# Optimization experiments

Measured on AMD Instinct MI355X. Metric: run time of the kernel, lower is better.

## Reference

```python
import jax, jax.numpy as jnp
import numpy as np

MASK_NEG = 1e30


def setup_inputs() -> dict:
    key = jax.random.key(0)
    k_q, k_k, k_m, k_w1, k_w2, k_v = jax.random.split(key, 6)
    B, S, D, A = 32, 2048, 1024, 1024  # batch, seq, feature dim, attn dim
    # Xavier-uniform-like scale for weights
    lim = float(np.sqrt(6.0 / (D + A)))
    query = jax.random.normal(k_q, (B, D), dtype=jnp.float32)
    keys = jax.random.normal(k_k, (B, S, D), dtype=jnp.float32)
    mask = jax.random.randint(k_m, (B, S), 0, 2) > 0  # True = keep
    W1 = jax.random.uniform(k_w1, (A, D), jnp.float32, -lim, lim)
    W2 = jax.random.uniform(k_w2, (A, D), jnp.float32, -lim, lim)
    v = jax.random.uniform(k_v, (A,), jnp.float32, -lim, lim)
    return {"query": query, "keys": keys, "mask": mask, "W1": W1, "W2": W2, "v": v}


def reference(query, keys, mask, W1, W2, v):
    w1_query = jnp.einsum('bd,ad->ba', query, W1)          # (B, A)
    w2_keys = jnp.einsum('bsd,ad->bsa', keys, W2)          # (B, S, A)
    combined = jnp.tanh(w1_query[:, None, :] + w2_keys)    # (B, S, A)
    scores = jnp.einsum('bsa,a->bs', combined, v)          # (B, S)
    # masked softmax: subtract huge constant at masked-out positions
    scores = scores - (~mask).astype(scores.dtype) * MASK_NEG
    return jax.nn.softmax(scores, axis=-1)
```

## Files before the change

kernel.cpp:

```cpp
#include <hip/hip_runtime.h>
#include <hip/hip_bf16.h>
#include <stdint.h>

#define NB 32
#define NS 2048
#define ND 1024
#define NA 1024
#define MASK_NEG 1e30f

#define BM 256
#define BN 256
#define BK 64
#define NTILES 64

typedef __attribute__((ext_vector_type(4))) float f32x4;
typedef __attribute__((ext_vector_type(8))) __bf16 bf16x8;

__device__ __forceinline__ void glds16(const void* g, void* l) {
  __builtin_amdgcn_global_load_lds(
      (const __attribute__((address_space(1))) uint32_t*)g,
      (__attribute__((address_space(3))) uint32_t*)(uintptr_t)l, 16, 0, 0);
}

__global__ void zero_f32(float* __restrict__ p, int n) {
  int i = blockIdx.x * 256 + threadIdx.x;
  if (i < n) p[i] = 0.f;
}

__global__ __launch_bounds__(256) void cvt_bf16(const float* __restrict__ in,
                                                __bf16* __restrict__ out, int n8) {
  long i = blockIdx.x * 256 + threadIdx.x;
  const long stride = (long)gridDim.x * 256;
  for (; i < n8; i += stride) {
    f32x4 a = ((const f32x4*)in)[2 * i];
    f32x4 b = ((const f32x4*)in)[2 * i + 1];
    bf16x8 o;
#pragma unroll
    for (int j = 0; j < 4; ++j) { o[j] = (__bf16)a[j]; o[4 + j] = (__bf16)b[j]; }
    ((bf16x8*)out)[i] = o;
  }
}

__global__ __launch_bounds__(256) void w1q_kernel(const float* __restrict__ q,
                                                  const float* __restrict__ W1,
                                                  float* __restrict__ w1q) {
  const int b = blockIdx.x;
  const int a0 = blockIdx.y * 64;
  const int t = threadIdx.x;
  const int al = t >> 2;
  const int part = t & 3;
  const float* wrow = W1 + (size_t)(a0 + al) * ND + part * 256;
  const float* qrow = q + (size_t)b * ND + part * 256;
  float sum = 0.f;
#pragma unroll 8
  for (int i = 0; i < 256; i += 4) {
    float4 w = *reinterpret_cast<const float4*>(wrow + i);
    float4 x = *reinterpret_cast<const float4*>(qrow + i);
    sum += w.x * x.x + w.y * x.y + w.z * x.z + w.w * x.w;
  }
  __shared__ float red[256];
  red[t] = sum;
  __syncthreads();
  if (t < 64) {
    w1q[(size_t)b * NA + a0 + t] = red[t * 4] + red[t * 4 + 1] + red[t * 4 + 2] + red[t * 4 + 3];
  }
}

__global__ __launch_bounds__(512, 1) void score_gemm(
    const float* __restrict__ keysf, const __bf16* __restrict__ W2b,
    const float* __restrict__ w1q, const float* __restrict__ vvec,
    float* __restrict__ scores) {
  __shared__ __attribute__((aligned(1024))) char ldsA[6 * 16384];
  __shared__ __attribute__((aligned(1024))) char ldsB[4 * 16384];

  const int t = threadIdx.x;
  const int bs0 = blockIdx.x * BM;
  const int b = bs0 >> 11;
  const int lane = t & 63;
  const int wid = t >> 6;
  const int wr = wid >> 2;
  const int wc = wid & 3;
  const int lrow = lane & 15;
  const int ko = lane >> 4;

  const int rowA = t >> 4;
  const int scolA = (t & 15) ^ (rowA & 15);
  const int rowB = t >> 3;
  const int scolB = (t & 7) ^ (rowB & 7);

  const int uA0 = ko * 2, uA1 = 8 + ko * 2;
  const int sA00 = uA0 ^ lrow, sA01 = (uA0 + 1) ^ lrow;
  const int sA10 = uA1 ^ lrow, sA11 = (uA1 + 1) ^ lrow;
  const int sB0 = ko ^ (lrow & 7), sB1 = (4 + ko) ^ (lrow & 7);

  f32x4 acc[8][4];
#pragma unroll
  for (int mi = 0; mi < 8; ++mi)
#pragma unroll
    for (int ni = 0; ni < 4; ++ni) acc[mi][ni] = f32x4{0.f, 0.f, 0.f, 0.f};

  bf16x8 af[4][2], bfr[2][2];

#define STAGE_A(T, Q)                                                           \
  do {                                                                          \
    if ((T) < NTILES) {                                                         \
      const unsigned slot_ = (4u * (unsigned)(T) + (unsigned)(Q)) % 6u;         \
      char* d_ = ldsA + slot_ * 16384 + t * 16;                                 \
      const size_t r0_ = (size_t)(bs0 + (Q)*64 + rowA);                         \
      const int kf_ = ((T)&15) * 64 + scolA * 4;                                \
      glds16(keysf + r0_ * ND + kf_, d_);                                       \
      glds16(keysf + (r0_ + 32) * ND + kf_, d_ + 8192);                         \
    }                                                                           \
  } while (0)

#define STAGE_B(T, H)                                                           \
  do {                                                                          \
    if ((T) < NTILES) {                                                         \
      const unsigned slot_ = (2u * (unsigned)(T) + (unsigned)(H)) % 4u;         \
      char* d_ = ldsB + slot_ * 16384 + t * 16;                                 \
      const size_t r0_ = (size_t)(((T) >> 4) * 256 + (H)*128 + rowB);           \
      const int ke_ = (((T)&15) * 64) + scolB * 8;                              \
      glds16(W2b + r0_ * ND + ke_, d_);                                         \
      glds16(W2b + (r0_ + 64) * ND + ke_, d_ + 8192);                           \
    }                                                                           \
  } while (0)

#define SB_ __builtin_amdgcn_sched_barrier(0)
#define P1 __builtin_amdgcn_s_setprio(1)
#define P0 __builtin_amdgcn_s_setprio(0)
#define BAR __builtin_amdgcn_s_barrier()

#define PHASE(M_, N_, STAGES, WM)                                               \
  do {                                                                          \
    STAGES;                                                                     \
    if ((N_) == 0) {                                                            \
      const char* Ab_ = ldsA + ((4u * (unsigned)tau + 2u * wr + (M_)) % 6u) * 16384; \
      _Pragma("unroll") for (int mi = 0; mi < 4; ++mi) {                        \
        const int rb_ = (mi * 16 + lrow) * 256;                                 \
        f32x4 l0 = *reinterpret_cast<const f32x4*>(Ab_ + rb_ + sA00 * 16);      \
        f32x4 l1 = *reinterpret_cast<const f32x4*>(Ab_ + rb_ + sA01 * 16);      \
        f32x4 h0 = *reinterpret_cast<const f32x4*>(Ab_ + rb_ + sA10 * 16);      \
        f32x4 h1 = *reinterpret_cast<const f32x4*>(Ab_ + rb_ + sA11 * 16);      \
        _Pragma("unroll") for (int j = 0; j < 4; ++j) {                         \
          af[mi][0][j] = (__bf16)l0[j]; af[mi][0][4 + j] = (__bf16)l1[j];       \
          af[mi][1][j] = (__bf16)h0[j]; af[mi][1][4 + j] = (__bf16)h1[j];       \
        }                                                                       \
      }                                                                         \
    }                                                                           \
    {                                                                           \
      const char* Bb_ = ldsB + ((2u * (unsigned)tau + (wc >> 1)) % 4u) * 16384; \
      _Pragma("unroll") for (int nq = 0; nq < 2; ++nq) {                        \
        const int rb_ = (((wc & 1) * 4 + (N_)*2 + nq) * 16 + lrow) * 128;       \
        bfr[nq][0] = *reinterpret_cast<const bf16x8*>(Bb_ + rb_ + sB0 * 16);    \
        bfr[nq][1] = *reinterpret_cast<const bf16x8*>(Bb_ + rb_ + sB1 * 16);    \
      }                                                                         \
    }                                                                           \
    BAR;                                                                        \
    asm volatile("s_waitcnt lgkmcnt(0)");                                       \
    SB_;                                                                        \
    P1;                                                                         \
    _Pragma("unroll") for (int mi = 0; mi < 4; ++mi)                            \
        _Pragma("unroll") for (int nq = 0; nq < 2; ++nq) {                      \
      acc[(M_)*4 + mi][(N_)*2 + nq] = __builtin_amdgcn_mfma_f32_16x16x32_bf16(  \
          af[mi][0], bfr[nq][0], acc[(M_)*4 + mi][(N_)*2 + nq], 0, 0, 0);       \
      acc[(M_)*4 + mi][(N_)*2 + nq] = __builtin_amdgcn_mfma_f32_16x16x32_bf16(  \
          af[mi][1], bfr[nq][1], acc[(M_)*4 + mi][(N_)*2 + nq], 0, 0, 0);       \
    }                                                                           \
    P0;                                                                         \
    if ((WM) == 1) {                                                            \
      if (tau < NTILES - 1) { asm volatile("s_waitcnt vmcnt(8)"); }             \
      else { asm volatile("s_waitcnt vmcnt(0)"); }                              \
      SB_;                                                                      \
    } else if ((WM) == 2) {                                                     \
      if (tau < NTILES - 1) { asm volatile("s_waitcnt vmcnt(4)"); SB_; }        \
    }                                                                           \
    BAR;                                                                        \
  } while (0)

  STAGE_A(0, 0);
  STAGE_A(0, 1);
  STAGE_A(0, 2);
  STAGE_A(0, 3);
  STAGE_B(0, 0);
  STAGE_B(0, 1);
  __syncthreads();

  for (int tau = 0; tau < NTILES; ++tau) {
    PHASE(0, 0, { STAGE_A(tau + 1, 0); STAGE_B(tau + 1, 0); }, 0);
    PHASE(0, 1, { STAGE_A(tau + 1, 2); STAGE_B(tau + 1, 1); }, 1);
    PHASE(1, 0, { STAGE_A(tau + 1, 1); }, 0);
    PHASE(1, 1, { STAGE_A(tau + 1, 3); }, 2);

    if ((tau & 15) == 15) {
      const int a0 = (tau >> 4) * BN;
      float w1v[4], vv[4];
#pragma unroll
      for (int ni = 0; ni < 4; ++ni) {
        const int a = a0 + wc * 64 + ni * 16 + lrow;
        w1v[ni] = w1q[(size_t)b * NA + a];
        vv[ni] = vvec[a];
      }
#pragma unroll
      for (int mi = 0; mi < 8; ++mi)
#pragma unroll
        for (int r = 0; r < 4; ++r) {
          float p = 0.f;
#pragma unroll
          for (int ni = 0; ni < 4; ++ni) {
            const float x = acc[mi][ni][r] + w1v[ni];
            const float e = __expf(2.f * x);
            p += (1.f - 2.f * __builtin_amdgcn_rcpf(e + 1.f)) * vv[ni];
          }
          p += __shfl_xor(p, 1);
          p += __shfl_xor(p, 2);
          p += __shfl_xor(p, 4);
          p += __shfl_xor(p, 8);
          if (lrow == 0)
            atomicAdd(&scores[bs0 + wr * 128 + mi * 16 + ko * 4 + r], p);
        }
#pragma unroll
      for (int mi = 0; mi < 8; ++mi)
#pragma unroll
        for (int ni = 0; ni < 4; ++ni) acc[mi][ni] = f32x4{0.f, 0.f, 0.f, 0.f};
    }
  }

#undef STAGE_A
#undef STAGE_B
#undef PHASE
#undef SB_
#undef P1
#undef P0
#undef BAR
}

__global__ __launch_bounds__(256) void softmax_kernel(const float* __restrict__ scores,
                                                      const int* __restrict__ mask,
                                                      float* __restrict__ out) {
  const int b = blockIdx.x;
  const int t = threadIdx.x;
  float sc[8];
  float mx = -3.4e38f;
#pragma unroll
  for (int j = 0; j < 8; ++j) {
    int i = t + j * 256;
    float s = scores[b * NS + i];
    if (mask[b * NS + i] == 0) s -= MASK_NEG;
    sc[j] = s;
    mx = fmaxf(mx, s);
  }
#pragma unroll
  for (int off = 1; off < 64; off <<= 1) mx = fmaxf(mx, __shfl_xor(mx, off));
  __shared__ float redm[4];
  __shared__ float reds[4];
  if ((t & 63) == 0) redm[t >> 6] = mx;
  __syncthreads();
  mx = fmaxf(fmaxf(redm[0], redm[1]), fmaxf(redm[2], redm[3]));
  float e[8];
  float sum = 0.f;
#pragma unroll
  for (int j = 0; j < 8; ++j) {
    e[j] = __expf(sc[j] - mx);
    sum += e[j];
  }
#pragma unroll
  for (int off = 1; off < 64; off <<= 1) sum += __shfl_xor(sum, off);
  if ((t & 63) == 0) reds[t >> 6] = sum;
  __syncthreads();
  sum = reds[0] + reds[1] + reds[2] + reds[3];
  float inv = 1.f / sum;
#pragma unroll
  for (int j = 0; j < 8; ++j) out[b * NS + t + j * 256] = e[j] * inv;
}

extern "C" void kernel_launch(void* const* d_in, const int* in_sizes, int n_in,
                              void* d_out, int out_size, void* d_ws, size_t ws_size,
                              hipStream_t stream) {
  const float* q = (const float*)d_in[0];
  const float* keysf = (const float*)d_in[1];
  const int* mask = (const int*)d_in[2];
  const float* W1 = (const float*)d_in[3];
  const float* W2f = (const float*)d_in[4];
  const float* v = (const float*)d_in[5];
  float* out = (float*)d_out;

  float* scores = (float*)d_ws;
  float* w1q = scores + NB * NS;
  __bf16* W2b = (__bf16*)(w1q + NB * NA);

  zero_f32<<<NB * NS / 256, 256, 0, stream>>>(scores, NB * NS);
  cvt_bf16<<<512, 256, 0, stream>>>(W2f, W2b, NA * ND / 8);
  w1q_kernel<<<dim3(NB, NA / 64), 256, 0, stream>>>(q, W1, w1q);
  score_gemm<<<NB * NS / BM, 512, 0, stream>>>(keysf, W2b, w1q, v, scores);
  softmax_kernel<<<NB, 256, 0, stream>>>(scores, mask, out);
}
```

Before: 236.3 us.

## Re-tile score GEMM waves to 4x2 grid with 64x128 per-wave tiles

Changes the wave layout from 2x4 (128 rows x 64 cols per wave) to 4x2 (64 rows x 128 cols per wave). Each wave now converts its A fragment from fp32 to bf16 once per K-tile instead of twice, and reads four B sub-tiles. The staging schedule is also reordered: all loads for the next tile are issued in the first two phases, with a single full vmcnt(0) wait at the end of the last phase. The intent is to cut LDS reads and fp32-to-bf16 conversions of A. The risk is less overlap between global loads and MFMA work, because the finer-grained partial waits are gone.

```diff
diff --git a/kernel.cpp b/kernel.cpp
--- a/kernel.cpp
+++ b/kernel.cpp
@@ -78,8 +78,8 @@
   const int b = bs0 >> 11;
   const int lane = t & 63;
   const int wid = t >> 6;
-  const int wr = wid >> 2;
-  const int wc = wid & 3;
+  const int wr = wid >> 1;
+  const int wc = wid & 1;
   const int lrow = lane & 15;
   const int ko = lane >> 4;
 
@@ -88,16 +88,15 @@
   const int rowB = t >> 3;
   const int scolB = (t & 7) ^ (rowB & 7);
 
-  const int uA0 = ko * 2, uA1 = 8 + ko * 2;
-  const int sA00 = uA0 ^ lrow, sA01 = (uA0 + 1) ^ lrow;
-  const int sA10 = uA1 ^ lrow, sA11 = (uA1 + 1) ^ lrow;
+  const int sA00 = (ko * 2) ^ lrow, sA01 = (ko * 2 + 1) ^ lrow;
+  const int sA10 = (8 + ko * 2) ^ lrow, sA11 = (8 + ko * 2 + 1) ^ lrow;
   const int sB0 = ko ^ (lrow & 7), sB1 = (4 + ko) ^ (lrow & 7);
 
-  f32x4 acc[8][4];
-#pragma unroll
-  for (int mi = 0; mi < 8; ++mi)
-#pragma unroll
-    for (int ni = 0; ni < 4; ++ni) acc[mi][ni] = f32x4{0.f, 0.f, 0.f, 0.f};
+  f32x4 acc[4][8];
+#pragma unroll
+  for (int mi = 0; mi < 4; ++mi)
+#pragma unroll
+    for (int ni = 0; ni < 8; ++ni) acc[mi][ni] = f32x4{0.f, 0.f, 0.f, 0.f};
 
   bf16x8 af[4][2], bfr[2][2];
 
@@ -130,11 +129,11 @@
 #define P0 __builtin_amdgcn_s_setprio(0)
 #define BAR __builtin_amdgcn_s_barrier()
 
-#define PHASE(M_, N_, STAGES, WM)                                               \
+#define PHASE(P_, STAGES)                                                       \
   do {                                                                          \
     STAGES;                                                                     \
-    if ((N_) == 0) {                                                            \
-      const char* Ab_ = ldsA + ((4u * (unsigned)tau + 2u * wr + (M_)) % 6u) * 16384; \
+    if ((P_) == 0) {                                                            \
+      const char* Ab_ = ldsA + ((4u * (unsigned)tau + (unsigned)wr) % 6u) * 16384; \
       _Pragma("unroll") for (int mi = 0; mi < 4; ++mi) {                        \
         const int rb_ = (mi * 16 + lrow) * 256;                                 \
         f32x4 l0 = *reinterpret_cast<const f32x4*>(Ab_ + rb_ + sA00 * 16);      \
@@ -148,9 +147,9 @@
       }                                                                         \
     }                                                                           \
     {                                                                           \
-      const char* Bb_ = ldsB + ((2u * (unsigned)tau + (wc >> 1)) % 4u) * 16384; \
+      const char* Bb_ = ldsB + ((2u * (unsigned)tau + (unsigned)wc) % 4u) * 16384; \
       _Pragma("unroll") for (int nq = 0; nq < 2; ++nq) {                        \
-        const int rb_ = (((wc & 1) * 4 + (N_)*2 + nq) * 16 + lrow) * 128;       \
+        const int rb_ = (((P_)*2 + nq) * 16 + lrow) * 128;                      \
         bfr[nq][0] = *reinterpret_cast<const bf16x8*>(Bb_ + rb_ + sB0 * 16);    \
         bfr[nq][1] = *reinterpret_cast<const bf16x8*>(Bb_ + rb_ + sB1 * 16);    \
       }                                                                         \
@@ -161,18 +160,15 @@
     P1;                                                                         \
     _Pragma("unroll") for (int mi = 0; mi < 4; ++mi)                            \
         _Pragma("unroll") for (int nq = 0; nq < 2; ++nq) {                      \
-      acc[(M_)*4 + mi][(N_)*2 + nq] = __builtin_amdgcn_mfma_f32_16x16x32_bf16(  \
-          af[mi][0], bfr[nq][0], acc[(M_)*4 + mi][(N_)*2 + nq], 0, 0, 0);       \
-      acc[(M_)*4 + mi][(N_)*2 + nq] = __builtin_amdgcn_mfma_f32_16x16x32_bf16(  \
-          af[mi][1], bfr[nq][1], acc[(M_)*4 + mi][(N_)*2 + nq], 0, 0, 0);       \
+      acc[mi][(P_)*2 + nq] = __builtin_amdgcn_mfma_f32_16x16x32_bf16(           \
+          af[mi][0], bfr[nq][0], acc[mi][(P_)*2 + nq], 0, 0, 0);                \
+      acc[mi][(P_)*2 + nq] = __builtin_amdgcn_mfma_f32_16x16x32_bf16(           \
+          af[mi][1], bfr[nq][1], acc[mi][(P_)*2 + nq], 0, 0, 0);                \
     }                                                                           \
     P0;                                                                         \
-    if ((WM) == 1) {                                                            \
-      if (tau < NTILES - 1) { asm volatile("s_waitcnt vmcnt(8)"); }             \
-      else { asm volatile("s_waitcnt vmcnt(0)"); }                              \
+    if ((P_) == 3) {                                                            \
+      asm volatile("s_waitcnt vmcnt(0)");                                       \
       SB_;                                                                      \
-    } else if ((WM) == 2) {                                                     \
-      if (tau < NTILES - 1) { asm volatile("s_waitcnt vmcnt(4)"); SB_; }        \
     }                                                                           \
     BAR;                                                                        \
   } while (0)
@@ -186,27 +182,27 @@
   __syncthreads();
 
   for (int tau = 0; tau < NTILES; ++tau) {
-    PHASE(0, 0, { STAGE_A(tau + 1, 0); STAGE_B(tau + 1, 0); }, 0);
-    PHASE(0, 1, { STAGE_A(tau + 1, 2); STAGE_B(tau + 1, 1); }, 1);
-    PHASE(1, 0, { STAGE_A(tau + 1, 1); }, 0);
-    PHASE(1, 1, { STAGE_A(tau + 1, 3); }, 2);
+    PHASE(0, { STAGE_A(tau + 1, 0); STAGE_A(tau + 1, 1); STAGE_B(tau + 1, 0); });
+    PHASE(1, { STAGE_A(tau + 1, 2); STAGE_A(tau + 1, 3); STAGE_B(tau + 1, 1); });
+    PHASE(2, {});
+    PHASE(3, {});
 
     if ((tau & 15) == 15) {
       const int a0 = (tau >> 4) * BN;
-      float w1v[4], vv[4];
-#pragma unroll
-      for (int ni = 0; ni < 4; ++ni) {
-        const int a = a0 + wc * 64 + ni * 16 + lrow;
+      float w1v[8], vv[8];
+#pragma unroll
+      for (int ni = 0; ni < 8; ++ni) {
+        const int a = a0 + wc * 128 + ni * 16 + lrow;
         w1v[ni] = w1q[(size_t)b * NA + a];
         vv[ni] = vvec[a];
       }
 #pragma unroll
-      for (int mi = 0; mi < 8; ++mi)
+      for (int mi = 0; mi < 4; ++mi)
 #pragma unroll
         for (int r = 0; r < 4; ++r) {
           float p = 0.f;
 #pragma unroll
-          for (int ni = 0; ni < 4; ++ni) {
+          for (int ni = 0; ni < 8; ++ni) {
             const float x = acc[mi][ni][r] + w1v[ni];
             const float e = __expf(2.f * x);
             p += (1.f - 2.f * __builtin_amdgcn_rcpf(e + 1.f)) * vv[ni];
@@ -216,12 +212,12 @@
           p += __shfl_xor(p, 4);
           p += __shfl_xor(p, 8);
           if (lrow == 0)
-            atomicAdd(&scores[bs0 + wr * 128 + mi * 16 + ko * 4 + r], p);
+            atomicAdd(&scores[bs0 + wr * 64 + mi * 16 + ko * 4 + r], p);
         }
 #pragma unroll
-      for (int mi = 0; mi < 8; ++mi)
-#pragma unroll
-        for (int ni = 0; ni < 4; ++ni) acc[mi][ni] = f32x4{0.f, 0.f, 0.f, 0.f};
+      for (int mi = 0; mi < 4; ++mi)
+#pragma unroll
+        for (int ni = 0; ni < 8; ++ni) acc[mi][ni] = f32x4{0.f, 0.f, 0.f, 0.f};
     }
   }
 
```

New measurement: 221.2 us. -6.4%, faster.
